# Kernel optimization log

Measured on AMD Instinct MI355X. Metric: run time of the kernel, lower is better.

## Reference

```python
import jax, jax.numpy as jnp
import numpy as np

N = 50000   # nodes
E = 800000  # edges
H = 3       # attention heads
IN_F = 128
HID = 128
NUM_CLASSES = 6
GAT_SLOPE = 0.2   # DGL GATConv internal leaky_relu slope
ACT_SLOPE = 0.01  # nn.LeakyReLU default


def setup_inputs() -> dict:
    key = jax.random.key(0)
    ks = jax.random.split(key, 24)
    s = 0.05
    inp = {
        "in_feat": jax.random.normal(ks[0], (N, IN_F), jnp.float32),
        "src": jax.random.randint(ks[1], (E,), 0, N, jnp.int32),
        "dst": jax.random.randint(ks[2], (E,), 0, N, jnp.int32),
        # GATConv 1: W (IN_F, H*HID), attn vectors (H, HID), bias (H*HID)
        "W1": jax.random.normal(ks[3], (IN_F, H * HID), jnp.float32) * s,
        "al1": jax.random.normal(ks[4], (H, HID), jnp.float32) * s,
        "ar1": jax.random.normal(ks[5], (H, HID), jnp.float32) * s,
        "b1": jnp.zeros((H * HID,), jnp.float32),
        # GATConv 2
        "W2": jax.random.normal(ks[6], (HID, H * HID), jnp.float32) * s,
        "al2": jax.random.normal(ks[7], (H, HID), jnp.float32) * s,
        "ar2": jax.random.normal(ks[8], (H, HID), jnp.float32) * s,
        "b2": jnp.zeros((H * HID,), jnp.float32),
    }
    # Dense MLP head lin1..lin4 (HID->HID) and lin5 (HID->NUM_CLASSES)
    for i in range(1, 5):
        inp[f"lw{i}"] = jax.random.normal(ks[8 + 2 * i], (HID, HID), jnp.float32) * s
        inp[f"lb{i}"] = jnp.zeros((HID,), jnp.float32)
    inp["lw5"] = jax.random.normal(ks[20], (HID, NUM_CLASSES), jnp.float32) * s
    inp["lb5"] = jnp.zeros((NUM_CLASSES,), jnp.float32)
    return inp


def gat_conv(x, src, dst, W, al, ar, b):
    # x: (N, F_in) -> out: (N, H, HID)
    h = (x @ W).reshape(N, H, HID)
    el = jnp.einsum('nhf,hf->nh', h, al)  # (N, H)
    er = jnp.einsum('nhf,hf->nh', h, ar)
    e = jax.nn.leaky_relu(el[src] + er[dst], GAT_SLOPE)  # (E, H)
    # edge softmax over incoming edges of each dst node
    m = jax.ops.segment_max(e, dst, num_segments=N)
    m = jnp.where(jnp.isfinite(m), m, 0.0)
    ex = jnp.exp(e - m[dst])
    denom = jax.ops.segment_sum(ex, dst, num_segments=N)
    alpha = ex / (denom[dst] + 1e-9)  # (E, H)
    out = jax.ops.segment_sum(alpha[:, :, None] * h[src], dst, num_segments=N)
    return out + b.reshape(1, H, HID)


def reference(in_feat, src, dst, W1, al1, ar1, b1, W2, al2, ar2, b2,
              lw1, lb1, lw2, lb2, lw3, lb3, lw4, lb4, lw5, lb5):
    act = lambda x: jax.nn.leaky_relu(x, ACT_SLOPE)
    h = act(gat_conv(in_feat, src, dst, W1, al1, ar1, b1)).mean(axis=1)
    h = act(gat_conv(h, src, dst, W2, al2, ar2, b2)).mean(axis=1)
    h = act(h @ lw1 + lb1)
    h = act(h @ lw2 + lb2)
    h = act(h @ lw3 + lb3)
    h = act(h @ lw4 + lb4)
    return h @ lw5 + lb5
```

## Files before the change

### kernel.cpp

```cpp
#include <hip/hip_runtime.h>
#include <hip/hip_bf16.h>


typedef __attribute__((ext_vector_type(8))) short short8;
typedef __attribute__((ext_vector_type(4))) float float4v;
typedef __attribute__((ext_vector_type(2))) float floatx2;

__device__ inline short f2bf(float x) {
    union { float f; unsigned u; } v; v.f = x;
    unsigned r = v.u + 0x7FFFu + ((v.u >> 16) & 1u);
    return (short)(r >> 16);
}
__device__ inline float bf2f(short b) {
    union { float f; unsigned u; } v;
    v.u = ((unsigned)(unsigned short)b) << 16;
    return v.f;
}
__device__ inline short8 zero8() { short8 z = {0,0,0,0,0,0,0,0}; return z; }

#if __has_builtin(__builtin_amdgcn_cvt_pk_fp8_f32)
__device__ inline unsigned short pk2fp8(float a, float b) {
    return (unsigned short)(__builtin_amdgcn_cvt_pk_fp8_f32(a, b, 0, false) & 0xFFFF);
}
#else
__device__ inline unsigned char f2fp8_1(float x) {
    union { float f; unsigned u; } v; v.f = x;
    unsigned s = (v.u >> 24) & 0x80u;
    unsigned au = v.u & 0x7FFFFFFFu;
    if (au >= 0x43E00000u) return (unsigned char)(s | 0x7E);
    if (au < 0x3C800000u) {
        union { float f; unsigned u; } a; a.u = au;
        int k = (int)(a.f * 512.0f + 0.5f);
        if (k > 7) return (unsigned char)(s | 0x08);
        return (unsigned char)(s | (unsigned)k);
    }
    unsigned r = au + 0x0007FFFFu + ((au >> 20) & 1u);
    unsigned e = (r >> 23) - 120u;
    unsigned m = (r >> 20) & 7u;
    if (e >= 15u && m >= 7u) { e = 15u; m = 6u; }
    return (unsigned char)(s | (e << 3) | m);
}
__device__ inline unsigned short pk2fp8(float a, float b) {
    return (unsigned short)f2fp8_1(a) | ((unsigned short)f2fp8_1(b) << 8);
}
#endif

#if __has_builtin(__builtin_amdgcn_cvt_pk_f32_fp8)
__device__ inline floatx2 unpk2fp8(unsigned short p) {
    return __builtin_amdgcn_cvt_pk_f32_fp8((int)p, false);
}
#else
__device__ inline float fp8_1_2f(unsigned char b) {
    unsigned s = b >> 7, e = (b >> 3) & 15u, m = b & 7u;
    float v = (e == 0) ? (float)m * 0.001953125f
                       : (float)(8u + m) * exp2f((float)((int)e - 10));
    return s ? -v : v;
}
__device__ inline floatx2 unpk2fp8(unsigned short p) {
    floatx2 r; r.x = fp8_1_2f((unsigned char)(p & 0xFF));
    r.y = fp8_1_2f((unsigned char)(p >> 8)); return r;
}
#endif

__device__ __forceinline__ void gl_lds16(const short* g, short* l) {
    __builtin_amdgcn_global_load_lds(
        (const __attribute__((address_space(1))) void*)g,
        (__attribute__((address_space(3))) void*)l,
        16, 0, 0);
}

#define SW(r) ((((r) >> 2) ^ (r)) & 3)

#define BM 128
#define BN 128
#define BK 32
#define MSTR 136
#define MROWS 64

__global__ void prep_kernel(
    const float* __restrict__ in_feat, short* __restrict__ P1h,
    short* __restrict__ P1l, int n4, int cb, int wb,
    const int* __restrict__ dst, int* __restrict__ cnt, int E,
    const float* __restrict__ w1, const float* __restrict__ w2,
    const float* __restrict__ m1, const float* __restrict__ m2,
    const float* __restrict__ m3, const float* __restrict__ m4,
    const float* __restrict__ w5,
    short* __restrict__ w1h, short* __restrict__ w1l,
    short* __restrict__ w2h, short* __restrict__ w2l,
    short* __restrict__ m1h, short* __restrict__ m1l,
    short* __restrict__ m2h, short* __restrict__ m2l,
    short* __restrict__ m3h, short* __restrict__ m3l,
    short* __restrict__ m4h, short* __restrict__ m4l,
    short* __restrict__ w5h, short* __restrict__ w5l)
{
    int blk = blockIdx.x;
    if (blk < cb) {
        int i = blk * 256 + threadIdx.x;
        if (i >= n4) return;
        float4 v = *(const float4*)(in_feat + (size_t)i * 4);
        float xs[4] = {v.x, v.y, v.z, v.w};
        short hs[4], ls[4];
        #pragma unroll
        for (int j = 0; j < 4; ++j) {
            hs[j] = f2bf(xs[j]);
            ls[j] = f2bf(xs[j] - bf2f(hs[j]));
        }
        *(uint2*)(P1h + (size_t)i * 4) = *(uint2*)hs;
        *(uint2*)(P1l + (size_t)i * 4) = *(uint2*)ls;
    } else if (blk < cb + wb) {
        int j = (blk - cb) * 256 + threadIdx.x;
        const float* src; short* th; short* tl; int Nc, base;
        if      (j < 49152)  { src = w1; th = w1h; tl = w1l; Nc = 384; base = 0; }
        else if (j < 98304)  { src = w2; th = w2h; tl = w2l; Nc = 384; base = 49152; }
        else if (j < 114688) { src = m1; th = m1h; tl = m1l; Nc = 128; base = 98304; }
        else if (j < 131072) { src = m2; th = m2h; tl = m2l; Nc = 128; base = 114688; }
        else if (j < 147456) { src = m3; th = m3h; tl = m3l; Nc = 128; base = 131072; }
        else if (j < 163840) { src = m4; th = m4h; tl = m4l; Nc = 128; base = 147456; }
        else if (j < 164608) { src = w5; th = w5h; tl = w5l; Nc = 6;   base = 163840; }
        else return;
        int i = j - base;
        int k = i / Nc, c = i - k * Nc;
        float v = src[i];
        short h = f2bf(v);
        th[(size_t)c * 128 + k] = h;
        tl[(size_t)c * 128 + k] = f2bf(v - bf2f(h));
    } else {
        int e = (blk - cb - wb) * 256 + threadIdx.x;
        if (e < E) atomicAdd(&cnt[dst[e]], 1);
    }
}

__global__ __launch_bounds__(256) void gemm_mfma(
    const short* __restrict__ Ahi, const short* __restrict__ Alo,
    const short* __restrict__ Bth, const short* __restrict__ Btl,
    const float* __restrict__ bias,
    float* __restrict__ Cf, short* __restrict__ Chi, short* __restrict__ Clo,
    unsigned char* __restrict__ Cf8,
    float* __restrict__ el, float* __restrict__ er,
    const float* __restrict__ al, const float* __restrict__ ar,
    int M, int Nc, int flags)
{
    __shared__ short Ah[BM * BK], Al_[BM * BK];
    __shared__ short Bh[BN * BK], Bl_[BN * BK];

    int tid = threadIdx.x, lane = tid & 63, wave = tid >> 6;
    int l15 = lane & 15, q = lane >> 4;
    int rowBase = blockIdx.y * BM, colBase = blockIdx.x * BN;

    float4v acc[2][8];
    #pragma unroll
    for (int mt = 0; mt < 2; ++mt)
        #pragma unroll
        for (int nt = 0; nt < 8; ++nt)
            acc[mt][nt] = (float4v){0.f, 0.f, 0.f, 0.f};

    for (int k0 = 0; k0 < 128; k0 += BK) {
        #pragma unroll
        for (int i = 0; i < 2; ++i) {
            int cid = tid + i * 256;
            int r = cid >> 2, sub = cid & 3;
            int gs = (sub ^ SW(r)) * 8;
            size_t ga = (size_t)(rowBase + r) * 128 + k0 + gs;
            size_t gb = (size_t)(colBase + r) * 128 + k0 + gs;
            int ld = cid * 8;
            gl_lds16(Ahi + ga, Ah  + ld);
            gl_lds16(Alo + ga, Al_ + ld);
            gl_lds16(Bth + gb, Bh  + ld);
            gl_lds16(Btl + gb, Bl_ + ld);
        }
        __syncthreads();

        short8 aH[2], aL2[2];
        #pragma unroll
        for (int mt = 0; mt < 2; ++mt) {
            int row = wave * 32 + mt * 16 + l15;
            int off = row * 32 + (q ^ SW(row)) * 8;
            aH[mt]  = *(short8*)&Ah[off];
            aL2[mt] = *(short8*)&Al_[off];
        }
        #pragma unroll
        for (int nt = 0; nt < 8; ++nt) {
            int row = nt * 16 + l15;
            int off = row * 32 + (q ^ SW(row)) * 8;
            short8 bH = *(short8*)&Bh[off];
            short8 bL = *(short8*)&Bl_[off];
            #pragma unroll
            for (int mt = 0; mt < 2; ++mt) {
                acc[mt][nt] = __builtin_amdgcn_mfma_f32_16x16x32_bf16(aH[mt], bH, acc[mt][nt], 0, 0, 0);
                acc[mt][nt] = __builtin_amdgcn_mfma_f32_16x16x32_bf16(aH[mt], bL, acc[mt][nt], 0, 0, 0);
                acc[mt][nt] = __builtin_amdgcn_mfma_f32_16x16x32_bf16(aL2[mt], bH, acc[mt][nt], 0, 0, 0);
            }
        }
        __syncthreads();
    }

    if (flags & 4) {
        const float* alh = al + colBase;
        const float* arh = ar + colBase;
        float pel[2][4] = {}, per_[2][4] = {};
        #pragma unroll
        for (int nt = 0; nt < 8; ++nt) {
            float av = alh[nt * 16 + l15];
            float rv = arh[nt * 16 + l15];
            #pragma unroll
            for (int mt = 0; mt < 2; ++mt)
                #pragma unroll
                for (int i = 0; i < 4; ++i) {
                    pel[mt][i]  += acc[mt][nt][i] * av;
                    per_[mt][i] += acc[mt][nt][i] * rv;
                }
        }
        #pragma unroll
        for (int mask = 1; mask < 16; mask <<= 1)
            #pragma unroll
            for (int mt = 0; mt < 2; ++mt)
                #pragma unroll
                for (int i = 0; i < 4; ++i) {
                    pel[mt][i]  += __shfl_xor(pel[mt][i], mask);
                    per_[mt][i] += __shfl_xor(per_[mt][i], mask);
                }
        if (l15 == 0) {
            #pragma unroll
            for (int mt = 0; mt < 2; ++mt)
                #pragma unroll
                for (int i = 0; i < 4; ++i) {
                    int r = rowBase + wave * 32 + mt * 16 + q * 4 + i;
                    if (r < M) {
                        el[r * 3 + blockIdx.x] = pel[mt][i];
                        er[r * 3 + blockIdx.x] = per_[mt][i];
                    }
                }
        }
    }

    #pragma unroll
    for (int mt = 0; mt < 2; ++mt) {
        #pragma unroll
        for (int nt = 0; nt < 8; ++nt) {
            int c = colBase + nt * 16 + l15;
            bool cok = c < Nc;
            float bv = ((flags & 1) && cok) ? bias[c] : 0.f;
            #pragma unroll
            for (int i = 0; i < 4; ++i) {
                int r = rowBase + wave * 32 + mt * 16 + q * 4 + i;
                float v = acc[mt][nt][i] + bv;
                if (flags & 2) v = (v < 0.f) ? 0.01f * v : v;
                float vn = __shfl_xor(v, 1);
                if (cok && r < M) {
                    size_t idx = (size_t)r * Nc + c;
                    if (flags & 8)  Cf[idx] = v;
                    if (flags & 16) {
                        short hh = f2bf(v);
                        Chi[idx] = hh;
                        if (flags & 32) Clo[idx] = f2bf(v - bf2f(hh));
                    }
                    if ((flags & 64) && !(l15 & 1))
                        *(unsigned short*)(Cf8 + idx) = pk2fp8(v, vn);
                }
            }
        }
    }
}

__global__ __launch_bounds__(256) void mlp_fused(
    const short* __restrict__ Ph, const short* __restrict__ Pl,
    const short* __restrict__ w1h, const short* __restrict__ w1l,
    const short* __restrict__ w2h, const short* __restrict__ w2l,
    const short* __restrict__ w3h, const short* __restrict__ w3l,
    const short* __restrict__ w4h, const short* __restrict__ w4l,
    const short* __restrict__ w5h, const short* __restrict__ w5l,
    const float* __restrict__ b1, const float* __restrict__ b2,
    const float* __restrict__ b3, const float* __restrict__ b4,
    const float* __restrict__ b5,
    float* __restrict__ out, int M)
{
    __shared__ short AH[MROWS * MSTR], AL[MROWS * MSTR];
    __shared__ short WH[128 * BK], WL[128 * BK];

    int tid = threadIdx.x, lane = tid & 63, wave = tid >> 6;
    int l15 = lane & 15, q = lane >> 4;
    int rowBase = blockIdx.x * MROWS;

    #pragma unroll
    for (int s = 0; s < 4; ++s) {
        int idx = tid + s * 256;
        int r = idx >> 4, kq = (idx & 15) * 8;
        int gr = rowBase + r;
        short8 vh = zero8(), vl = zero8();
        if (gr < M) {
            vh = *(const short8*)(Ph + (size_t)gr * 128 + kq);
            vl = *(const short8*)(Pl + (size_t)gr * 128 + kq);
        }
        *(short8*)&AH[r * MSTR + kq] = vh;
        *(short8*)&AL[r * MSTR + kq] = vl;
    }

    const short* Whs[4] = {w1h, w2h, w3h, w4h};
    const short* Wls[4] = {w1l, w2l, w3l, w4l};
    const float* Bss[4] = {b1, b2, b3, b4};

    #pragma unroll
    for (int L = 0; L < 4; ++L) {
        float4v acc[8];
        #pragma unroll
        for (int nt = 0; nt < 8; ++nt)
            acc[nt] = (float4v){0.f, 0.f, 0.f, 0.f};

        for (int k0 = 0; k0 < 128; k0 += BK) {
            #pragma unroll
            for (int i = 0; i < 4; ++i) {
                int c2 = tid + (i & 1) * 256;
                int r = c2 >> 2, sub = c2 & 3;
                int gs = (sub ^ SW(r)) * 8;
                if (i < 2) gl_lds16(Whs[L] + (size_t)r * 128 + k0 + gs, WH + c2 * 8);
                else       gl_lds16(Wls[L] + (size_t)r * 128 + k0 + gs, WL + c2 * 8);
            }
            __syncthreads();
            int offa = (wave * 16 + l15) * MSTR + k0 + q * 8;
            short8 aH  = *(short8*)&AH[offa];
            short8 aL2 = *(short8*)&AL[offa];
            #pragma unroll
            for (int nt = 0; nt < 8; ++nt) {
                int row = nt * 16 + l15;
                int off = row * 32 + (q ^ SW(row)) * 8;
                short8 bH = *(short8*)&WH[off];
                short8 bL = *(short8*)&WL[off];
                acc[nt] = __builtin_amdgcn_mfma_f32_16x16x32_bf16(aH, bH, acc[nt], 0, 0, 0);
                acc[nt] = __builtin_amdgcn_mfma_f32_16x16x32_bf16(aH, bL, acc[nt], 0, 0, 0);
                acc[nt] = __builtin_amdgcn_mfma_f32_16x16x32_bf16(aL2, bH, acc[nt], 0, 0, 0);
            }
            __syncthreads();
        }
        #pragma unroll
        for (int nt = 0; nt < 8; ++nt) {
            int c = nt * 16 + l15;
            float bv = Bss[L][c];
            #pragma unroll
            for (int i = 0; i < 4; ++i) {
                int r = wave * 16 + q * 4 + i;
                float v = acc[nt][i] + bv;
                v = (v < 0.f) ? 0.01f * v : v;
                short hh = f2bf(v);
                AH[r * MSTR + c] = hh;
                AL[r * MSTR + c] = f2bf(v - bf2f(hh));
            }
        }
        __syncthreads();
    }

    float4v acc5 = (float4v){0.f, 0.f, 0.f, 0.f};
    for (int k0 = 0; k0 < 128; k0 += BK) {
        if (tid < 128) {
            int plane = tid >> 6, rem = tid & 63;
            int c = rem >> 2, sub = rem & 3;
            short8 v = zero8();
            if (c < 6)
                v = *(const short8*)((plane ? w5l : w5h) + (size_t)c * 128 + k0 + sub * 8);
            *(short8*)&((plane ? WL : WH)[c * 32 + (sub ^ SW(c)) * 8]) = v;
        }
        __syncthreads();
        int offa = (wave * 16 + l15) * MSTR + k0 + q * 8;
        short8 aH  = *(short8*)&AH[offa];
        short8 aL2 = *(short8*)&AL[offa];
        int offb = l15 * 32 + (q ^ SW(l15)) * 8;
        short8 bH = *(short8*)&WH[offb];
        short8 bL = *(short8*)&WL[offb];
        acc5 = __builtin_amdgcn_mfma_f32_16x16x32_bf16(aH, bH, acc5, 0, 0, 0);
        acc5 = __builtin_amdgcn_mfma_f32_16x16x32_bf16(aH, bL, acc5, 0, 0, 0);
        acc5 = __builtin_amdgcn_mfma_f32_16x16x32_bf16(aL2, bH, acc5, 0, 0, 0);
        __syncthreads();
    }
    if (l15 < 6) {
        float bv = b5[l15];
        #pragma unroll
        for (int i = 0; i < 4; ++i) {
            int r = rowBase + wave * 16 + q * 4 + i;
            if (r < M) out[(size_t)r * 6 + l15] = acc5[i] + bv;
        }
    }
}

__global__ __launch_bounds__(1024) void scan_block(const int* __restrict__ cnt,
                                                   int* __restrict__ off,
                                                   int* __restrict__ bsum, int n)
{
    __shared__ int tmp[1024];
    int tid = threadIdx.x;
    int i = blockIdx.x * 1024 + tid;
    int v = (i < n) ? cnt[i] : 0;
    tmp[tid] = v;
    __syncthreads();
    for (int s = 1; s < 1024; s <<= 1) {
        int t = (tid >= s) ? tmp[tid - s] : 0;
        __syncthreads();
        tmp[tid] += t;
        __syncthreads();
    }
    if (i < n) off[i] = tmp[tid] - v;
    if (tid == 1023) bsum[blockIdx.x] = tmp[1023];
}

__global__ void scan_add2(int* __restrict__ off, const int* __restrict__ bsum,
                          int n, int nb)
{
    __shared__ int pre[64];
    int tid = threadIdx.x;
    if (tid < 64) {
        int v = (tid < nb) ? bsum[tid] : 0;
        #pragma unroll
        for (int s = 1; s < 64; s <<= 1) {
            int t = __shfl_up(v, s);
            if (tid >= s) v += t;
        }
        pre[tid] = v;
    }
    __syncthreads();
    int i = blockIdx.x * blockDim.x + tid;
    if (i < n) {
        int chunk = i >> 10;
        off[i] += chunk ? pre[chunk - 1] : 0;
    }
    if (i == 0) off[n] = pre[nb - 1];
}

__global__ void scatter_kernel(const int* __restrict__ src, const int* __restrict__ dst,
                               const int* __restrict__ off, int* __restrict__ cnt,
                               int* __restrict__ csrc, int E)
{
    int e = blockIdx.x * blockDim.x + threadIdx.x;
    if (e < E) {
        int d = dst[e];
        int p = atomicSub(&cnt[d], 1) - 1;
        csrc[off[d] + p] = src[e];
    }
}

template <bool FP8>
__global__ __launch_bounds__(192) void agg_kernel(
    const void* __restrict__ hsrc, const float* __restrict__ el,
    const float* __restrict__ er, const int* __restrict__ off,
    const int* __restrict__ csrc, const float* __restrict__ bias,
    short* __restrict__ outH, short* __restrict__ outL, int N)
{
    const unsigned char* h8 = (const unsigned char*)hsrc;
    const short*         hb = (const short*)hsrc;
    int n = blockIdx.x;
    int tid = threadIdx.x;
    int head = tid >> 6;
    int l = tid & 63;
    int beg = off[n], end = off[n + 1];
    int deg = end - beg;

    __shared__ int   ssrc[64];
    __shared__ float sw[3][64];
    __shared__ float sm[384];

    int fbase = head * 128 + 2 * l;
    float erv = er[n * 3 + head];
    float ax = 0.f, ay = 0.f, den = 0.f, m_run = -1e30f;

    for (int base = 0; base < deg; base += 64) {
        int cnt = min(64, deg - base);
        if (tid < cnt) ssrc[tid] = csrc[beg + base + tid];
        __syncthreads();
        float e = -1e30f;
        if (l < cnt) {
            float t = el[ssrc[l] * 3 + head] + erv;
            e = (t < 0.f) ? 0.2f * t : t;
        }
        float mc = e;
        #pragma unroll
        for (int msk = 1; msk < 64; msk <<= 1) mc = fmaxf(mc, __shfl_xor(mc, msk));
        float m_new = fmaxf(m_run, mc);
        float scale = __expf(m_run - m_new);
        ax *= scale; ay *= scale; den *= scale;
        float w = (l < cnt) ? __expf(e - m_new) : 0.f;
        float wsum = w;
        #pragma unroll
        for (int msk = 1; msk < 64; msk <<= 1) wsum += __shfl_xor(wsum, msk);
        den += wsum;
        sw[head][l] = w;
        m_run = m_new;
        #pragma unroll 4
        for (int qq = 0; qq < cnt; ++qq) {
            int s = ssrc[qq];
            float w2 = sw[head][qq];
            if (FP8) {
                unsigned short v = *(const unsigned short*)(h8 + (size_t)s * 384 + fbase);
                floatx2 f = unpk2fp8(v);
                ax += w2 * f.x;
                ay += w2 * f.y;
            } else {
                unsigned v = *(const unsigned*)(hb + (size_t)s * 384 + fbase);
                union { unsigned u; float f; } f0, f1;
                f0.u = v << 16; f1.u = v & 0xffff0000u;
                ax += w2 * f0.f;
                ay += w2 * f1.f;
            }
        }
        __syncthreads();
    }
    float r = 1.f / (den + 1e-9f);
    if (deg == 0) r = 0.f;
    float2 bv = *(const float2*)(bias + fbase);
    float vx = ax * r + bv.x; vx = (vx < 0.f) ? 0.01f * vx : vx;
    float vy = ay * r + bv.y; vy = (vy < 0.f) ? 0.01f * vy : vy;
    sm[fbase]     = vx;
    sm[fbase + 1] = vy;
    __syncthreads();
    if (tid < 64) {
        int f0i = tid * 2, f1i = f0i + 1;
        float mx = (sm[f0i] + sm[128 + f0i] + sm[256 + f0i]) * (1.0f / 3.0f);
        float my = (sm[f1i] + sm[128 + f1i] + sm[256 + f1i]) * (1.0f / 3.0f);
        short hx = f2bf(mx), lx = f2bf(mx - bf2f(hx));
        short hy = f2bf(my), ly = f2bf(my - bf2f(hy));
        unsigned ph = (unsigned)(unsigned short)hx | ((unsigned)(unsigned short)hy << 16);
        unsigned pl = (unsigned)(unsigned short)lx | ((unsigned)(unsigned short)ly << 16);
        *(unsigned*)(outH + (size_t)n * 128 + f0i) = ph;
        *(unsigned*)(outL + (size_t)n * 128 + f0i) = pl;
    }
}

extern "C" void kernel_launch(void* const* d_in, const int* in_sizes, int n_in,
                              void* d_out, int out_size, void* d_ws, size_t ws_size,
                              hipStream_t stream)
{
    const float* in_feat = (const float*)d_in[0];
    const int*   src     = (const int*)d_in[1];
    const int*   dst     = (const int*)d_in[2];
    const float* W1  = (const float*)d_in[3];
    const float* al1 = (const float*)d_in[4];
    const float* ar1 = (const float*)d_in[5];
    const float* b1  = (const float*)d_in[6];
    const float* W2  = (const float*)d_in[7];
    const float* al2 = (const float*)d_in[8];
    const float* ar2 = (const float*)d_in[9];
    const float* b2  = (const float*)d_in[10];
    const float* lw1 = (const float*)d_in[11];
    const float* lb1 = (const float*)d_in[12];
    const float* lw2 = (const float*)d_in[13];
    const float* lb2 = (const float*)d_in[14];
    const float* lw3 = (const float*)d_in[15];
    const float* lb3 = (const float*)d_in[16];
    const float* lw4 = (const float*)d_in[17];
    const float* lb4 = (const float*)d_in[18];
    const float* lw5 = (const float*)d_in[19];
    const float* lb5 = (const float*)d_in[20];

    const int N = in_sizes[0] / 128;
    const int E = in_sizes[1];

    size_t o = 0;
    auto alloc = [&](size_t bytes) { size_t p = o; o = (o + bytes + 255) & ~(size_t)255; return p; };
    char* ws = (char*)d_ws;
    short* P1h = (short*)(ws + alloc((size_t)N * 128 * 2));
    short* P1l = (short*)(ws + alloc((size_t)N * 128 * 2));
    short* P2h = (short*)(ws + alloc((size_t)N * 128 * 2));
    short* P2l = (short*)(ws + alloc((size_t)N * 128 * 2));
    short* AbH = (short*)(ws + alloc((size_t)N * 384 * 2));
    unsigned char* Af8 = (unsigned char*)(ws + alloc((size_t)N * 384));
    float* el  = (float*)(ws + alloc((size_t)N * 3 * 4));
    float* er  = (float*)(ws + alloc((size_t)N * 3 * 4));
    int*   cnt  = (int*)(ws + alloc((size_t)N * 4));
    int*   off  = (int*)(ws + alloc((size_t)(N + 1) * 4));
    int*   bsum = (int*)(ws + alloc((size_t)4096));
    int*   csrc = (int*)(ws + alloc((size_t)E * 4));
    short* w1th = (short*)(ws + alloc((size_t)384 * 128 * 2));
    short* w1tl = (short*)(ws + alloc((size_t)384 * 128 * 2));
    short* w2th = (short*)(ws + alloc((size_t)384 * 128 * 2));
    short* w2tl = (short*)(ws + alloc((size_t)384 * 128 * 2));
    short* l1th = (short*)(ws + alloc((size_t)128 * 128 * 2));
    short* l1tl = (short*)(ws + alloc((size_t)128 * 128 * 2));
    short* l2th = (short*)(ws + alloc((size_t)128 * 128 * 2));
    short* l2tl = (short*)(ws + alloc((size_t)128 * 128 * 2));
    short* l3th = (short*)(ws + alloc((size_t)128 * 128 * 2));
    short* l3tl = (short*)(ws + alloc((size_t)128 * 128 * 2));
    short* l4th = (short*)(ws + alloc((size_t)128 * 128 * 2));
    short* l4tl = (short*)(ws + alloc((size_t)128 * 128 * 2));
    short* l5th = (short*)(ws + alloc((size_t)6 * 128 * 2));
    short* l5tl = (short*)(ws + alloc((size_t)6 * 128 * 2));
    (void)ws_size;

    float* out = (float*)d_out;

    hipMemsetAsync(cnt, 0, (size_t)N * 4, stream);
    int n4 = N * 128 / 4;
    int cb = (n4 + 255) / 256;
    int wb = (164608 + 255) / 256;
    int hb = (E + 255) / 256;
    prep_kernel<<<cb + wb + hb, 256, 0, stream>>>(
        in_feat, P1h, P1l, n4, cb, wb, dst, cnt, E,
        W1, W2, lw1, lw2, lw3, lw4, lw5,
        w1th, w1tl, w2th, w2tl, l1th, l1tl, l2th, l2tl,
        l3th, l3tl, l4th, l4tl, l5th, l5tl);

    int nb = (N + 1023) / 1024;
    scan_block<<<nb, 1024, 0, stream>>>(cnt, off, bsum, N);
    scan_add2<<<(N + 255) / 256, 256, 0, stream>>>(off, bsum, N, nb);
    scatter_kernel<<<(E + 255) / 256, 256, 0, stream>>>(src, dst, off, cnt, csrc, E);

    int RB = (N + BM - 1) / BM;
    auto gemm = [&](const short* ah, const short* alo, const short* bth, const short* btl,
                    const float* bias, float* cf, short* chi, short* clo,
                    unsigned char* cf8,
                    float* elp, float* erp, const float* alp, const float* arp,
                    int Nc, int flags) {
        dim3 grid((Nc + BN - 1) / BN, RB);
        gemm_mfma<<<grid, 256, 0, stream>>>(ah, alo, bth, btl, bias, cf, chi, clo, cf8,
                                            elp, erp, alp, arp, N, Nc, flags);
    };

    gemm(P1h, P1l, w1th, w1tl, nullptr, nullptr, nullptr, nullptr, Af8, el, er, al1, ar1, 384, 4 | 64);
    agg_kernel<true><<<N, 192, 0, stream>>>(Af8, el, er, off, csrc, b1, P2h, P2l, N);

    gemm(P2h, P2l, w2th, w2tl, nullptr, nullptr, AbH, nullptr, nullptr, el, er, al2, ar2, 384, 4 | 16);
    agg_kernel<false><<<N, 192, 0, stream>>>(AbH, el, er, off, csrc, b2, P1h, P1l, N);

    int RBM = (N + MROWS - 1) / MROWS;
    mlp_fused<<<RBM, 256, 0, stream>>>(P1h, P1l,
                                       l1th, l1tl, l2th, l2tl, l3th, l3tl,
                                       l4th, l4tl, l5th, l5tl,
                                       lb1, lb2, lb3, lb4, lb5, out, N);
}
```

Baseline: 524.6 us.

## Use 16-byte vector gathers per lane across multiple edges in GAT aggregation

Each wavefront now spreads its 64 lanes over several edges at once: each lane loads 16 contiguous bytes of a neighbor's head segment, giving 8 (FP8) or 4 (bf16) edges per iteration instead of one. Per-lane partial sums are then combined across edge groups with xor shuffles before normalisation and bias. This replaces narrow 2–4 byte gathers with wide loads and cuts loop trip count, aiming to improve memory-level parallelism in the gather-bound aggregation. It adds more accumulator registers and a final shuffle reduction, and pads the source list with node 0 so out-of-range slots read harmless data with zero weight.

```diff
diff --git a/kernel.cpp b/kernel.cpp
--- a/kernel.cpp
+++ b/kernel.cpp
@@ -442,12 +442,19 @@
     const int* __restrict__ csrc, const float* __restrict__ bias,
     short* __restrict__ outH, short* __restrict__ outL, int N)
 {
-    const unsigned char* h8 = (const unsigned char*)hsrc;
-    const short*         hb = (const short*)hsrc;
+    constexpr int RPL  = FP8 ? 8 : 4;
+    constexpr int LPR  = 64 / RPL;
+    constexpr int FPL  = 128 / LPR;
+    constexpr int ROWB = FP8 ? 384 : 768;
+    constexpr int SEGB = ROWB / 3;
+
+    const unsigned char* hb = (const unsigned char*)hsrc;
     int n = blockIdx.x;
     int tid = threadIdx.x;
     int head = tid >> 6;
     int l = tid & 63;
+    int rg = l / LPR;
+    int fi = l & (LPR - 1);
     int beg = off[n], end = off[n + 1];
     int deg = end - beg;
 
@@ -455,13 +462,16 @@
     __shared__ float sw[3][64];
     __shared__ float sm[384];
 
-    int fbase = head * 128 + 2 * l;
+    float acc[FPL];
+    #pragma unroll
+    for (int k = 0; k < FPL; ++k) acc[k] = 0.f;
+    float den = 0.f, m_run = -1e30f;
     float erv = er[n * 3 + head];
-    float ax = 0.f, ay = 0.f, den = 0.f, m_run = -1e30f;
+    const unsigned char* hseg = hb + head * SEGB + fi * 16;
 
     for (int base = 0; base < deg; base += 64) {
         int cnt = min(64, deg - base);
-        if (tid < cnt) ssrc[tid] = csrc[beg + base + tid];
+        if (tid < 64) ssrc[tid] = (base + tid < deg) ? csrc[beg + base + tid] : 0;
         __syncthreads();
         float e = -1e30f;
         if (l < cnt) {
@@ -473,7 +483,9 @@
         for (int msk = 1; msk < 64; msk <<= 1) mc = fmaxf(mc, __shfl_xor(mc, msk));
         float m_new = fmaxf(m_run, mc);
         float scale = __expf(m_run - m_new);
-        ax *= scale; ay *= scale; den *= scale;
+        #pragma unroll
+        for (int k = 0; k < FPL; ++k) acc[k] *= scale;
+        den *= scale;
         float w = (l < cnt) ? __expf(e - m_new) : 0.f;
         float wsum = w;
         #pragma unroll
@@ -481,32 +493,50 @@
         den += wsum;
         sw[head][l] = w;
         m_run = m_new;
-        #pragma unroll 4
-        for (int qq = 0; qq < cnt; ++qq) {
-            int s = ssrc[qq];
-            float w2 = sw[head][qq];
-            if (FP8) {
-                unsigned short v = *(const unsigned short*)(h8 + (size_t)s * 384 + fbase);
-                floatx2 f = unpk2fp8(v);
-                ax += w2 * f.x;
-                ay += w2 * f.y;
+        #pragma unroll 2
+        for (int j = 0; j < cnt; j += RPL) {
+            int e2 = j + rg;
+            int s = ssrc[e2];
+            float wv = sw[head][e2];
+            union { uint4 u4; unsigned u[4]; unsigned short us[8]; } uv;
+            uv.u4 = *(const uint4*)(hseg + (size_t)s * ROWB);
+            if constexpr (FP8) {
+                #pragma unroll
+                for (int t = 0; t < 8; ++t) {
+                    floatx2 f = unpk2fp8(uv.us[t]);
+                    acc[2 * t]     += wv * f.x;
+                    acc[2 * t + 1] += wv * f.y;
+                }
             } else {
-                unsigned v = *(const unsigned*)(hb + (size_t)s * 384 + fbase);
-                union { unsigned u; float f; } f0, f1;
-                f0.u = v << 16; f1.u = v & 0xffff0000u;
-                ax += w2 * f0.f;
-                ay += w2 * f1.f;
+                #pragma unroll
+                for (int t = 0; t < 4; ++t) {
+                    union { unsigned u; float f; } f0, f1;
+                    f0.u = uv.u[t] << 16; f1.u = uv.u[t] & 0xffff0000u;
+                    acc[2 * t]     += wv * f0.f;
+                    acc[2 * t + 1] += wv * f1.f;
+                }
             }
         }
         __syncthreads();
     }
+
+    #pragma unroll
+    for (int msk = LPR; msk < 64; msk <<= 1)
+        #pragma unroll
+        for (int k = 0; k < FPL; ++k)
+            acc[k] += __shfl_xor(acc[k], msk);
+
     float r = 1.f / (den + 1e-9f);
     if (deg == 0) r = 0.f;
-    float2 bv = *(const float2*)(bias + fbase);
-    float vx = ax * r + bv.x; vx = (vx < 0.f) ? 0.01f * vx : vx;
-    float vy = ay * r + bv.y; vy = (vy < 0.f) ? 0.01f * vy : vy;
-    sm[fbase]     = vx;
-    sm[fbase + 1] = vy;
+    if (rg == 0) {
+        int fb = head * 128 + fi * FPL;
+        #pragma unroll
+        for (int k = 0; k < FPL; ++k) {
+            float v = acc[k] * r + bias[fb + k];
+            v = (v < 0.f) ? 0.01f * v : v;
+            sm[fb + k] = v;
+        }
+    }
     __syncthreads();
     if (tid < 64) {
         int f0i = tid * 2, f1i = f0i + 1;
```

Result: slower. 588.9 us (+12.3%).

## Restructure GAT aggregation: two nodes per block, batched gathers, no block syncs

Applied to the files above, without the earlier changes.

The aggregation kernel now handles two destination nodes per 384-thread block, and each wave owns private shared-memory slots, so the per-chunk __syncthreads calls go away. The online running-max softmax is replaced by plain exp accumulation. The denominator is reduced once at the end instead of per chunk. Neighbor feature gathers are issued in batches of eight independent loads to raise memory-level parallelism. The trade-off is that dropping the max subtraction gives up overflow protection for large attention logits.

```diff
diff --git a/kernel.cpp b/kernel.cpp
--- a/kernel.cpp
+++ b/kernel.cpp
@@ -436,88 +436,111 @@
 }
 
 template <bool FP8>
-__global__ __launch_bounds__(192) void agg_kernel(
+__global__ __launch_bounds__(384) void agg_kernel(
     const void* __restrict__ hsrc, const float* __restrict__ el,
     const float* __restrict__ er, const int* __restrict__ off,
     const int* __restrict__ csrc, const float* __restrict__ bias,
     short* __restrict__ outH, short* __restrict__ outL, int N)
 {
-    const unsigned char* h8 = (const unsigned char*)hsrc;
-    const short*         hb = (const short*)hsrc;
-    int n = blockIdx.x;
+    constexpr int ROWB = FP8 ? 384 : 768;
+    constexpr int SEGB = ROWB / 3;
+
+    const unsigned char* hb = (const unsigned char*)hsrc;
     int tid = threadIdx.x;
-    int head = tid >> 6;
+    int u = tid >> 6;
+    int nl = u / 3;
+    int head = u - nl * 3;
     int l = tid & 63;
-    int beg = off[n], end = off[n + 1];
-    int deg = end - beg;
-
-    __shared__ int   ssrc[64];
-    __shared__ float sw[3][64];
-    __shared__ float sm[384];
-
-    int fbase = head * 128 + 2 * l;
-    float erv = er[n * 3 + head];
-    float ax = 0.f, ay = 0.f, den = 0.f, m_run = -1e30f;
+    int n = blockIdx.x * 2 + nl;
+    bool active = (n < N);
+
+    __shared__ int   ssrcS[6][64];
+    __shared__ float swS[6][64];
+    __shared__ float smS[2][384];
+
+    int beg = 0, deg = 0;
+    float erv = 0.f;
+    if (active) {
+        beg = off[n];
+        deg = off[n + 1] - beg;
+        erv = er[n * 3 + head];
+    }
+
+    const unsigned char* hseg = hb + head * SEGB + l * (FP8 ? 2 : 4);
+    float ax = 0.f, ay = 0.f, denl = 0.f;
 
     for (int base = 0; base < deg; base += 64) {
         int cnt = min(64, deg - base);
-        if (tid < cnt) ssrc[tid] = csrc[beg + base + tid];
-        __syncthreads();
-        float e = -1e30f;
+        int s_l = 0; float w = 0.f;
         if (l < cnt) {
-            float t = el[ssrc[l] * 3 + head] + erv;
-            e = (t < 0.f) ? 0.2f * t : t;
-        }
-        float mc = e;
-        #pragma unroll
-        for (int msk = 1; msk < 64; msk <<= 1) mc = fmaxf(mc, __shfl_xor(mc, msk));
-        float m_new = fmaxf(m_run, mc);
-        float scale = __expf(m_run - m_new);
-        ax *= scale; ay *= scale; den *= scale;
-        float w = (l < cnt) ? __expf(e - m_new) : 0.f;
-        float wsum = w;
-        #pragma unroll
-        for (int msk = 1; msk < 64; msk <<= 1) wsum += __shfl_xor(wsum, msk);
-        den += wsum;
-        sw[head][l] = w;
-        m_run = m_new;
-        #pragma unroll 4
-        for (int qq = 0; qq < cnt; ++qq) {
-            int s = ssrc[qq];
-            float w2 = sw[head][qq];
-            if (FP8) {
-                unsigned short v = *(const unsigned short*)(h8 + (size_t)s * 384 + fbase);
-                floatx2 f = unpk2fp8(v);
-                ax += w2 * f.x;
-                ay += w2 * f.y;
-            } else {
-                unsigned v = *(const unsigned*)(hb + (size_t)s * 384 + fbase);
-                union { unsigned u; float f; } f0, f1;
-                f0.u = v << 16; f1.u = v & 0xffff0000u;
-                ax += w2 * f0.f;
-                ay += w2 * f1.f;
-            }
-        }
-        __syncthreads();
-    }
+            s_l = csrc[beg + base + l];
+            float t = el[s_l * 3 + head] + erv;
+            t = (t < 0.f) ? 0.2f * t : t;
+            w = __expf(t);
+        }
+        denl += w;
+        ssrcS[u][l] = s_l;
+        swS[u][l]   = w;
+        for (int q0 = 0; q0 < cnt; q0 += 8) {
+            int sA[8]; float wA[8]; unsigned vA[8];
+            #pragma unroll
+            for (int b = 0; b < 8; ++b) {
+                int e = q0 + b;
+                sA[b] = ssrcS[u][e];
+                wA[b] = swS[u][e];
+            }
+            #pragma unroll
+            for (int b = 0; b < 8; ++b) {
+                if constexpr (FP8)
+                    vA[b] = *(const unsigned short*)(hseg + (size_t)sA[b] * ROWB);
+                else
+                    vA[b] = *(const unsigned*)(hseg + (size_t)sA[b] * ROWB);
+            }
+            #pragma unroll
+            for (int b = 0; b < 8; ++b) {
+                if constexpr (FP8) {
+                    floatx2 f = unpk2fp8((unsigned short)vA[b]);
+                    ax += wA[b] * f.x;
+                    ay += wA[b] * f.y;
+                } else {
+                    union { unsigned u; float f; } f0, f1;
+                    f0.u = vA[b] << 16; f1.u = vA[b] & 0xffff0000u;
+                    ax += wA[b] * f0.f;
+                    ay += wA[b] * f1.f;
+                }
+            }
+        }
+    }
+
+    float den = denl;
+    #pragma unroll
+    for (int msk = 1; msk < 64; msk <<= 1) den += __shfl_xor(den, msk);
     float r = 1.f / (den + 1e-9f);
     if (deg == 0) r = 0.f;
-    float2 bv = *(const float2*)(bias + fbase);
-    float vx = ax * r + bv.x; vx = (vx < 0.f) ? 0.01f * vx : vx;
-    float vy = ay * r + bv.y; vy = (vy < 0.f) ? 0.01f * vy : vy;
-    sm[fbase]     = vx;
-    sm[fbase + 1] = vy;
+
+    if (active) {
+        int fb = head * 128 + 2 * l;
+        float2 bv = *(const float2*)(bias + fb);
+        float vx = ax * r + bv.x; vx = (vx < 0.f) ? 0.01f * vx : vx;
+        float vy = ay * r + bv.y; vy = (vy < 0.f) ? 0.01f * vy : vy;
+        smS[nl][fb]     = vx;
+        smS[nl][fb + 1] = vy;
+    }
     __syncthreads();
-    if (tid < 64) {
-        int f0i = tid * 2, f1i = f0i + 1;
-        float mx = (sm[f0i] + sm[128 + f0i] + sm[256 + f0i]) * (1.0f / 3.0f);
-        float my = (sm[f1i] + sm[128 + f1i] + sm[256 + f1i]) * (1.0f / 3.0f);
-        short hx = f2bf(mx), lx = f2bf(mx - bf2f(hx));
-        short hy = f2bf(my), ly = f2bf(my - bf2f(hy));
-        unsigned ph = (unsigned)(unsigned short)hx | ((unsigned)(unsigned short)hy << 16);
-        unsigned pl = (unsigned)(unsigned short)lx | ((unsigned)(unsigned short)ly << 16);
-        *(unsigned*)(outH + (size_t)n * 128 + f0i) = ph;
-        *(unsigned*)(outL + (size_t)n * 128 + f0i) = pl;
+    if (tid < 128) {
+        int mn = tid >> 6;
+        int n2 = blockIdx.x * 2 + mn;
+        if (n2 < N) {
+            int f0i = (tid & 63) * 2, f1i = f0i + 1;
+            float mx = (smS[mn][f0i] + smS[mn][128 + f0i] + smS[mn][256 + f0i]) * (1.0f / 3.0f);
+            float my = (smS[mn][f1i] + smS[mn][128 + f1i] + smS[mn][256 + f1i]) * (1.0f / 3.0f);
+            short hx = f2bf(mx), lx = f2bf(mx - bf2f(hx));
+            short hy = f2bf(my), ly = f2bf(my - bf2f(hy));
+            unsigned ph = (unsigned)(unsigned short)hx | ((unsigned)(unsigned short)hy << 16);
+            unsigned pl = (unsigned)(unsigned short)lx | ((unsigned)(unsigned short)ly << 16);
+            *(unsigned*)(outH + (size_t)n2 * 128 + f0i) = ph;
+            *(unsigned*)(outL + (size_t)n2 * 128 + f0i) = pl;
+        }
     }
 }
 
@@ -610,11 +633,12 @@
                                             elp, erp, alp, arp, N, Nc, flags);
     };
 
+    int AGB = (N + 1) / 2;
     gemm(P1h, P1l, w1th, w1tl, nullptr, nullptr, nullptr, nullptr, Af8, el, er, al1, ar1, 384, 4 | 64);
-    agg_kernel<true><<<N, 192, 0, stream>>>(Af8, el, er, off, csrc, b1, P2h, P2l, N);
+    agg_kernel<true><<<AGB, 384, 0, stream>>>(Af8, el, er, off, csrc, b1, P2h, P2l, N);
 
     gemm(P2h, P2l, w2th, w2tl, nullptr, nullptr, AbH, nullptr, nullptr, el, er, al2, ar2, 384, 4 | 16);
-    agg_kernel<false><<<N, 192, 0, stream>>>(AbH, el, er, off, csrc, b2, P1h, P1l, N);
+    agg_kernel<false><<<AGB, 384, 0, stream>>>(AbH, el, er, off, csrc, b2, P1h, P1l, N);
 
     int RBM = (N + MROWS - 1) / MROWS;
     mlp_fused<<<RBM, 256, 0, stream>>>(P1h, P1l,
```

New measurement: 520.7 us. No clear change (-0.7%).
